# Performance work log

Hardware: AMD Instinct MI355X
Metric: run time of the kernel (lower is better)

Reference implementation:

```python
import jax, jax.numpy as jnp
import numpy as np

N = 50000      # number of predictions
E = 1_600_000  # total neighborhood entries (sum of neighborhood sizes)
D = 128        # prediction representation dim
A = 4          # additional per-pair info dim (box offsets / IoU)
H = 128        # block hidden dim


def setup_inputs() -> dict:
    key = jax.random.key(0)
    ks = jax.random.split(key, 16)
    interpolated = jax.random.normal(ks[0], (N, D), dtype=jnp.float32)
    add_info = jax.random.normal(ks[1], (E, A), dtype=jnp.float32)
    neighbor_idx = jax.random.randint(ks[2], (E,), 0, N, dtype=jnp.int32)
    segment_ids = jnp.sort(jax.random.randint(ks[3], (E,), 0, N, dtype=jnp.int32))
    w = lambda k, shape: (jax.random.normal(k, shape, dtype=jnp.float32) * 0.02)
    return {
        "interpolated": interpolated,
        "add_info": add_info,
        "neighbor_idx": neighbor_idx,
        "segment_ids": segment_ids,
        "Wb0": w(ks[4], (D + A, H)), "bb0": jnp.zeros((H,), jnp.float32),
        "Wo0": w(ks[5], (H, D)),     "bo0": jnp.zeros((D,), jnp.float32),
        "Wb1": w(ks[6], (D + A, H)), "bb1": jnp.zeros((H,), jnp.float32),
        "Wo1": w(ks[7], (H, D)),     "bo1": jnp.zeros((D,), jnp.float32),
        "Wf": w(ks[8], (D, 1)),      "bf": jnp.zeros((1,), jnp.float32),
    }


def reference(interpolated, add_info, neighbor_idx, segment_ids,
              Wb0, bb0, Wo0, bo0, Wb1, bb1, Wo1, bo1, Wf, bf):
    def block_step(feats, Wb, bb, Wo, bo):
        # assemble all neighborhoods: gather neighbor reps, concat pair info -> (E, D+A)
        edge_feats = jnp.concatenate([feats[neighbor_idx], add_info], axis=-1)
        # block MLP on neighborhood entries -> (E, H)
        h = jax.nn.relu(edge_feats @ Wb + bb)
        # segment-wise max pool over each prediction's neighborhood -> (N, H)
        pooled = jax.ops.segment_max(h, segment_ids, num_segments=N)
        pooled = jnp.where(jnp.isfinite(pooled), pooled, 0.0)  # empty segments -> 0
        # output projection back to representation space, residual update
        return feats + (pooled @ Wo + bo)

    x = block_step(interpolated, Wb0, bb0, Wo0, bo0)
    x = block_step(x, Wb1, bb1, Wo1, bo1)
    # final layers: compress representation to updated objectness score -> (N, 1)
    return x @ Wf + bf
```

## Files before the change

### kernel.cpp

```cpp
#include <hip/hip_runtime.h>
#include <limits.h>
#include <cstdint>

typedef __bf16 bf16_t;
typedef __attribute__((ext_vector_type(8))) __bf16 bf16x8;
typedef __attribute__((ext_vector_type(4))) float f32x4;
typedef __attribute__((ext_vector_type(2))) float f32x2;

#define CH 64

__device__ __forceinline__ float rlf(float v, int l) {
  return __int_as_float(__builtin_amdgcn_readlane(__float_as_int(v), l));
}

struct PackArgs {
  const float* W[4];
  bf16_t* P[4];
};

__global__ __launch_bounds__(256) void pack4_kernel(PackArgs args) {
  int idx = blockIdx.x * blockDim.x + threadIdx.x;
  int which = idx >> 14;
  int r = idx & 16383;
  int j  = r & 7;
  int L  = (r >> 3) & 63;
  int nt = (r >> 9) & 7;
  int kt = r >> 12;
  int k = kt * 32 + (L >> 4) * 8 + j;
  int n = nt * 16 + (L & 15);
  args.P[which][r] = (bf16_t)args.W[which][(size_t)k * 128 + n];
}

__global__ __launch_bounds__(256, 4) void yproj_f32(
    const float* __restrict__ X, const bf16_t* __restrict__ Wtpk,
    bf16_t* __restrict__ Ybf, float* __restrict__ pooled, int N)
{
  const int tid = threadIdx.x;
  const int base = blockIdx.x * 128;

  float4 z = make_float4(0.f, 0.f, 0.f, 0.f);
  #pragma unroll
  for (int i = 0; i < 16; ++i) {
    int idx = tid + i * 256;
    int row = base + (idx >> 5);
    if (row < N)
      reinterpret_cast<float4*>(pooled)[(size_t)row * 32 + (idx & 31)] = z;
  }

  const int lane = tid & 63;
  const int w    = tid >> 6;
  const int q    = lane >> 4;
  const int ln   = lane & 15;
  const int n0   = base + w * 32;

  int r0 = n0 + ln, r1 = n0 + 16 + ln;
  int r0c = (r0 < N) ? r0 : (N - 1);
  int r1c = (r1 < N) ? r1 : (N - 1);
  const float* x0 = X + (size_t)r0c * 128 + q * 8;
  const float* x1 = X + (size_t)r1c * 128 + q * 8;

  f32x4 acc[2][8];
  #pragma unroll
  for (int mt = 0; mt < 2; ++mt)
    #pragma unroll
    for (int nt = 0; nt < 8; ++nt)
      #pragma unroll
      for (int r = 0; r < 4; ++r) acc[mt][nt][r] = 0.f;

  const bf16x8* Wp = reinterpret_cast<const bf16x8*>(Wtpk);
  #pragma unroll
  for (int kt = 0; kt < 4; ++kt) {
    float4 f0a = *reinterpret_cast<const float4*>(x0 + kt * 32);
    float4 f0b = *reinterpret_cast<const float4*>(x0 + kt * 32 + 4);
    float4 f1a = *reinterpret_cast<const float4*>(x1 + kt * 32);
    float4 f1b = *reinterpret_cast<const float4*>(x1 + kt * 32 + 4);
    bf16x8 a0, a1;
    a0[0] = (bf16_t)f0a.x; a0[1] = (bf16_t)f0a.y; a0[2] = (bf16_t)f0a.z; a0[3] = (bf16_t)f0a.w;
    a0[4] = (bf16_t)f0b.x; a0[5] = (bf16_t)f0b.y; a0[6] = (bf16_t)f0b.z; a0[7] = (bf16_t)f0b.w;
    a1[0] = (bf16_t)f1a.x; a1[1] = (bf16_t)f1a.y; a1[2] = (bf16_t)f1a.z; a1[3] = (bf16_t)f1a.w;
    a1[4] = (bf16_t)f1b.x; a1[5] = (bf16_t)f1b.y; a1[6] = (bf16_t)f1b.z; a1[7] = (bf16_t)f1b.w;
    #pragma unroll
    for (int nt = 0; nt < 8; ++nt) {
      bf16x8 bfrag = Wp[(kt * 8 + nt) * 64 + lane];
      acc[0][nt] = __builtin_amdgcn_mfma_f32_16x16x32_bf16(a0, bfrag, acc[0][nt], 0, 0, 0);
      acc[1][nt] = __builtin_amdgcn_mfma_f32_16x16x32_bf16(a1, bfrag, acc[1][nt], 0, 0, 0);
    }
  }

  #pragma unroll
  for (int mt = 0; mt < 2; ++mt) {
    #pragma unroll
    for (int r = 0; r < 4; ++r) {
      int row = n0 + mt * 16 + q * 4 + r;
      if (row < N) {
        #pragma unroll
        for (int nt = 0; nt < 8; ++nt) {
          int col = nt * 16 + ln;
          Ybf[(size_t)row * 128 + col] = (bf16_t)acc[mt][nt][r];
        }
      }
    }
  }
}

__global__ __launch_bounds__(256, 4) void yproj_bf16(
    const bf16_t* __restrict__ Xbf, const bf16_t* __restrict__ Wtpk,
    bf16_t* __restrict__ Ybf, float* __restrict__ pooled, int N)
{
  const int tid = threadIdx.x;
  const int base = blockIdx.x * 128;

  float4 z = make_float4(0.f, 0.f, 0.f, 0.f);
  #pragma unroll
  for (int i = 0; i < 16; ++i) {
    int idx = tid + i * 256;
    int row = base + (idx >> 5);
    if (row < N)
      reinterpret_cast<float4*>(pooled)[(size_t)row * 32 + (idx & 31)] = z;
  }

  const int lane = tid & 63;
  const int w    = tid >> 6;
  const int q    = lane >> 4;
  const int ln   = lane & 15;
  const int n0   = base + w * 32;

  int r0 = n0 + ln, r1 = n0 + 16 + ln;
  int r0c = (r0 < N) ? r0 : (N - 1);
  int r1c = (r1 < N) ? r1 : (N - 1);
  const bf16_t* x0 = Xbf + (size_t)r0c * 128 + q * 8;
  const bf16_t* x1 = Xbf + (size_t)r1c * 128 + q * 8;

  f32x4 acc[2][8];
  #pragma unroll
  for (int mt = 0; mt < 2; ++mt)
    #pragma unroll
    for (int nt = 0; nt < 8; ++nt)
      #pragma unroll
      for (int r = 0; r < 4; ++r) acc[mt][nt][r] = 0.f;

  const bf16x8* Wp = reinterpret_cast<const bf16x8*>(Wtpk);
  #pragma unroll
  for (int kt = 0; kt < 4; ++kt) {
    bf16x8 a0 = *reinterpret_cast<const bf16x8*>(x0 + kt * 32);
    bf16x8 a1 = *reinterpret_cast<const bf16x8*>(x1 + kt * 32);
    #pragma unroll
    for (int nt = 0; nt < 8; ++nt) {
      bf16x8 bfrag = Wp[(kt * 8 + nt) * 64 + lane];
      acc[0][nt] = __builtin_amdgcn_mfma_f32_16x16x32_bf16(a0, bfrag, acc[0][nt], 0, 0, 0);
      acc[1][nt] = __builtin_amdgcn_mfma_f32_16x16x32_bf16(a1, bfrag, acc[1][nt], 0, 0, 0);
    }
  }

  #pragma unroll
  for (int mt = 0; mt < 2; ++mt) {
    #pragma unroll
    for (int r = 0; r < 4; ++r) {
      int row = n0 + mt * 16 + q * 4 + r;
      if (row < N) {
        #pragma unroll
        for (int nt = 0; nt < 8; ++nt) {
          int col = nt * 16 + ln;
          Ybf[(size_t)row * 128 + col] = (bf16_t)acc[mt][nt][r];
        }
      }
    }
  }
}

__global__ __launch_bounds__(256) void edge_stream(
    const bf16_t* __restrict__ Y,
    const float* __restrict__ Wb,
    const float* __restrict__ bb,
    const float* __restrict__ add_info,
    const int* __restrict__ nbr, const int* __restrict__ segs,
    float* __restrict__ pooled, int E)
{
  const int lane = threadIdx.x & 63;
  const int wv = __builtin_amdgcn_readfirstlane(threadIdx.x >> 6);
  const int e0 = (blockIdx.x * 4 + wv) * CH;
  if (e0 >= E) return;
  const int c0 = lane * 2;

  f32x2 wk[4];
  #pragma unroll
  for (int k = 0; k < 4; ++k) {
    wk[k].x = Wb[(size_t)(128 + k) * 128 + c0];
    wk[k].y = Wb[(size_t)(128 + k) * 128 + c0 + 1];
  }
  f32x2 bbv;
  bbv.x = bb[c0]; bbv.y = bb[c0 + 1];

  unsigned* pooled_u = reinterpret_cast<unsigned*>(pooled);
  f32x2 v; v.x = 0.f; v.y = 0.f;

  if (e0 + CH <= E) {
    int v_nbr = nbr[e0 + lane];
    int v_sg  = segs[e0 + lane];
    float v_ai[4];
    #pragma unroll
    for (int r = 0; r < 4; ++r)
      v_ai[r] = add_info[(size_t)e0 * 4 + r * 64 + lane];

    int cur = __builtin_amdgcn_readlane(v_sg, 0);

    unsigned ybuf[4][8];
    #pragma unroll
    for (int p = 0; p < 3; ++p) {
      #pragma unroll
      for (int j = 0; j < 8; ++j) {
        int rn = __builtin_amdgcn_readlane(v_nbr, p * 8 + j);
        ybuf[p][j] = *((const unsigned*)(Y + (size_t)rn * 128) + lane);
      }
    }

    #pragma unroll
    for (int g = 0; g < CH / 8; ++g) {
      if (g + 3 < CH / 8) {
        #pragma unroll
        for (int j = 0; j < 8; ++j) {
          int rn = __builtin_amdgcn_readlane(v_nbr, (g + 3) * 8 + j);
          ybuf[(g + 3) & 3][j] = *((const unsigned*)(Y + (size_t)rn * 128) + lane);
        }
      }
      #pragma unroll
      for (int j = 0; j < 8; ++j) {
        const int i = g * 8 + j;
        int sg = __builtin_amdgcn_readlane(v_sg, i);
        if (sg != cur) {
          if (v.x > 0.f) atomicMax(&pooled_u[(size_t)cur * 128 + c0], __float_as_uint(v.x));
          if (v.y > 0.f) atomicMax(&pooled_u[(size_t)cur * 128 + c0 + 1], __float_as_uint(v.y));
          v.x = 0.f; v.y = 0.f; cur = sg;
        }
        unsigned yb = ybuf[g & 3][j];
        f32x2 y;
        y.x = __uint_as_float(yb << 16);
        y.y = __uint_as_float(yb & 0xffff0000u);
        float a0 = rlf(v_ai[i >> 4], (i * 4 + 0) & 63);
        float a1 = rlf(v_ai[i >> 4], (i * 4 + 1) & 63);
        float a2 = rlf(v_ai[i >> 4], (i * 4 + 2) & 63);
        float a3 = rlf(v_ai[i >> 4], (i * 4 + 3) & 63);
        f32x2 t = bbv + a0 * wk[0];
        t += a1 * wk[1];
        t += a2 * wk[2];
        t += a3 * wk[3];
        t += y;
        v = __builtin_elementwise_max(v, t);
      }
    }
    if (v.x > 0.f) atomicMax(&pooled_u[(size_t)cur * 128 + c0], __float_as_uint(v.x));
    if (v.y > 0.f) atomicMax(&pooled_u[(size_t)cur * 128 + c0 + 1], __float_as_uint(v.y));
  } else {
    int cur = segs[e0];
    const int rem = E - e0;
    for (int i = 0; i < rem; ++i) {
      const int e = e0 + i;
      int sg = segs[e];
      if (sg != cur) {
        if (v.x > 0.f) atomicMax(&pooled_u[(size_t)cur * 128 + c0], __float_as_uint(v.x));
        if (v.y > 0.f) atomicMax(&pooled_u[(size_t)cur * 128 + c0 + 1], __float_as_uint(v.y));
        v.x = 0.f; v.y = 0.f; cur = sg;
      }
      unsigned yb = *reinterpret_cast<const unsigned*>(Y + (size_t)nbr[e] * 128 + c0);
      float y0 = __uint_as_float(yb << 16);
      float y1 = __uint_as_float(yb & 0xffff0000u);
      const float* ai = add_info + (size_t)e * 4;
      float a0 = ai[0], a1 = ai[1], a2 = ai[2], a3 = ai[3];
      float t0 = y0 + bbv.x + a0 * wk[0].x + a1 * wk[1].x + a2 * wk[2].x + a3 * wk[3].x;
      float t1 = y1 + bbv.y + a0 * wk[0].y + a1 * wk[1].y + a2 * wk[2].y + a3 * wk[3].y;
      v.x = fmaxf(v.x, t0);
      v.y = fmaxf(v.y, t1);
    }
    if (v.x > 0.f) atomicMax(&pooled_u[(size_t)cur * 128 + c0], __float_as_uint(v.x));
    if (v.y > 0.f) atomicMax(&pooled_u[(size_t)cur * 128 + c0 + 1], __float_as_uint(v.y));
  }
}

__global__ __launch_bounds__(256, 4) void update_mfma(
    const float* __restrict__ featsIn, const float* __restrict__ pooled,
    const bf16_t* __restrict__ Wopk, const float* __restrict__ bo,
    float* __restrict__ featsOut, bf16_t* __restrict__ featsOutBf, int N)
{
  const int tid  = threadIdx.x;
  const int lane = tid & 63;
  const int w    = tid >> 6;
  const int q    = lane >> 4;
  const int ln   = lane & 15;
  const int n0   = blockIdx.x * 128 + w * 32;

  int r0 = n0 + ln, r1 = n0 + 16 + ln;
  int r0c = (r0 < N) ? r0 : (N - 1);
  int r1c = (r1 < N) ? r1 : (N - 1);
  const float* p0 = pooled + (size_t)r0c * 128 + q * 8;
  const float* p1 = pooled + (size_t)r1c * 128 + q * 8;

  f32x4 acc[2][8];
  #pragma unroll
  for (int mt = 0; mt < 2; ++mt)
    #pragma unroll
    for (int nt = 0; nt < 8; ++nt)
      #pragma unroll
      for (int r = 0; r < 4; ++r) acc[mt][nt][r] = 0.f;

  const bf16x8* Wp = reinterpret_cast<const bf16x8*>(Wopk);
  #pragma unroll
  for (int kt = 0; kt < 4; ++kt) {
    float4 f0a = *reinterpret_cast<const float4*>(p0 + kt * 32);
    float4 f0b = *reinterpret_cast<const float4*>(p0 + kt * 32 + 4);
    float4 f1a = *reinterpret_cast<const float4*>(p1 + kt * 32);
    float4 f1b = *reinterpret_cast<const float4*>(p1 + kt * 32 + 4);
    bf16x8 a0, a1;
    a0[0] = (bf16_t)f0a.x; a0[1] = (bf16_t)f0a.y; a0[2] = (bf16_t)f0a.z; a0[3] = (bf16_t)f0a.w;
    a0[4] = (bf16_t)f0b.x; a0[5] = (bf16_t)f0b.y; a0[6] = (bf16_t)f0b.z; a0[7] = (bf16_t)f0b.w;
    a1[0] = (bf16_t)f1a.x; a1[1] = (bf16_t)f1a.y; a1[2] = (bf16_t)f1a.z; a1[3] = (bf16_t)f1a.w;
    a1[4] = (bf16_t)f1b.x; a1[5] = (bf16_t)f1b.y; a1[6] = (bf16_t)f1b.z; a1[7] = (bf16_t)f1b.w;
    #pragma unroll
    for (int nt = 0; nt < 8; ++nt) {
      bf16x8 bfrag = Wp[(kt * 8 + nt) * 64 + lane];
      acc[0][nt] = __builtin_amdgcn_mfma_f32_16x16x32_bf16(a0, bfrag, acc[0][nt], 0, 0, 0);
      acc[1][nt] = __builtin_amdgcn_mfma_f32_16x16x32_bf16(a1, bfrag, acc[1][nt], 0, 0, 0);
    }
  }

  float bov[8];
  #pragma unroll
  for (int nt = 0; nt < 8; ++nt) bov[nt] = bo[nt * 16 + ln];

  #pragma unroll
  for (int mt = 0; mt < 2; ++mt) {
    #pragma unroll
    for (int r = 0; r < 4; ++r) {
      int row = n0 + mt * 16 + q * 4 + r;
      if (row < N) {
        #pragma unroll
        for (int nt = 0; nt < 8; ++nt) {
          int col = nt * 16 + ln;
          float o = featsIn[(size_t)row * 128 + col] + acc[mt][nt][r] + bov[nt];
          featsOut[(size_t)row * 128 + col] = o;
          featsOutBf[(size_t)row * 128 + col] = (bf16_t)o;
        }
      }
    }
  }
}

__global__ __launch_bounds__(256, 4) void update_final_mfma(
    const float* __restrict__ featsIn, const float* __restrict__ pooled,
    const bf16_t* __restrict__ Wopk, const float* __restrict__ bo,
    const float* __restrict__ Wf, const float* __restrict__ bf_,
    float* __restrict__ out, int N)
{
  const int tid  = threadIdx.x;
  const int lane = tid & 63;
  const int w    = tid >> 6;
  const int q    = lane >> 4;
  const int ln   = lane & 15;
  const int n0   = blockIdx.x * 128 + w * 32;

  int r0 = n0 + ln, r1 = n0 + 16 + ln;
  int r0c = (r0 < N) ? r0 : (N - 1);
  int r1c = (r1 < N) ? r1 : (N - 1);
  const float* p0 = pooled + (size_t)r0c * 128 + q * 8;
  const float* p1 = pooled + (size_t)r1c * 128 + q * 8;

  f32x4 acc[2][8];
  #pragma unroll
  for (int mt = 0; mt < 2; ++mt)
    #pragma unroll
    for (int nt = 0; nt < 8; ++nt)
      #pragma unroll
      for (int r = 0; r < 4; ++r) acc[mt][nt][r] = 0.f;

  const bf16x8* Wp = reinterpret_cast<const bf16x8*>(Wopk);
  #pragma unroll
  for (int kt = 0; kt < 4; ++kt) {
    float4 f0a = *reinterpret_cast<const float4*>(p0 + kt * 32);
    float4 f0b = *reinterpret_cast<const float4*>(p0 + kt * 32 + 4);
    float4 f1a = *reinterpret_cast<const float4*>(p1 + kt * 32);
    float4 f1b = *reinterpret_cast<const float4*>(p1 + kt * 32 + 4);
    bf16x8 a0, a1;
    a0[0] = (bf16_t)f0a.x; a0[1] = (bf16_t)f0a.y; a0[2] = (bf16_t)f0a.z; a0[3] = (bf16_t)f0a.w;
    a0[4] = (bf16_t)f0b.x; a0[5] = (bf16_t)f0b.y; a0[6] = (bf16_t)f0b.z; a0[7] = (bf16_t)f0b.w;
    a1[0] = (bf16_t)f1a.x; a1[1] = (bf16_t)f1a.y; a1[2] = (bf16_t)f1a.z; a1[3] = (bf16_t)f1a.w;
    a1[4] = (bf16_t)f1b.x; a1[5] = (bf16_t)f1b.y; a1[6] = (bf16_t)f1b.z; a1[7] = (bf16_t)f1b.w;
    #pragma unroll
    for (int nt = 0; nt < 8; ++nt) {
      bf16x8 bfrag = Wp[(kt * 8 + nt) * 64 + lane];
      acc[0][nt] = __builtin_amdgcn_mfma_f32_16x16x32_bf16(a0, bfrag, acc[0][nt], 0, 0, 0);
      acc[1][nt] = __builtin_amdgcn_mfma_f32_16x16x32_bf16(a1, bfrag, acc[1][nt], 0, 0, 0);
    }
  }

  float bov[8], wfv[8];
  #pragma unroll
  for (int nt = 0; nt < 8; ++nt) { bov[nt] = bo[nt * 16 + ln]; wfv[nt] = Wf[nt * 16 + ln]; }
  float bfs = bf_[0];

  #pragma unroll
  for (int mt = 0; mt < 2; ++mt) {
    #pragma unroll
    for (int r = 0; r < 4; ++r) {
      int row = n0 + mt * 16 + q * 4 + r;
      float partial = 0.f;
      if (row < N) {
        #pragma unroll
        for (int nt = 0; nt < 8; ++nt) {
          int col = nt * 16 + ln;
          float o = featsIn[(size_t)row * 128 + col] + acc[mt][nt][r] + bov[nt];
          partial += o * wfv[nt];
        }
      }
      partial += __shfl_xor(partial, 1);
      partial += __shfl_xor(partial, 2);
      partial += __shfl_xor(partial, 4);
      partial += __shfl_xor(partial, 8);
      if (ln == 0 && row < N) out[row] = partial + bfs;
    }
  }
}

extern "C" void kernel_launch(void* const* d_in, const int* in_sizes, int n_in,
                              void* d_out, int out_size, void* d_ws, size_t ws_size,
                              hipStream_t stream)
{
  const float* interpolated = (const float*)d_in[0];
  const float* add_info     = (const float*)d_in[1];
  const int*   nbr          = (const int*)d_in[2];
  const int*   segs         = (const int*)d_in[3];
  const float* Wb0 = (const float*)d_in[4];
  const float* bb0 = (const float*)d_in[5];
  const float* Wo0 = (const float*)d_in[6];
  const float* bo0 = (const float*)d_in[7];
  const float* Wb1 = (const float*)d_in[8];
  const float* bb1 = (const float*)d_in[9];
  const float* Wo1 = (const float*)d_in[10];
  const float* bo1 = (const float*)d_in[11];
  const float* Wf  = (const float*)d_in[12];
  const float* bf_ = (const float*)d_in[13];

  const int N = in_sizes[0] / 128;
  const int E = in_sizes[2];
  float* out = (float*)d_out;

  float* pooled = (float*)d_ws;
  float* featsB = pooled + (size_t)N * 128;
  bf16_t* featsB_bf = (bf16_t*)(featsB + (size_t)N * 128);
  bf16_t* Ybf       = featsB_bf + (size_t)N * 128;
  bf16_t* Wtpk0 = Ybf + (size_t)N * 128;
  bf16_t* Wtpk1 = Wtpk0 + 16384;
  bf16_t* Wopk0 = Wtpk1 + 16384;
  bf16_t* Wopk1 = Wopk0 + 16384;

  const int ugrid = (N + 127) / 128;
  const int egrid = (E + CH * 4 - 1) / (CH * 4);

  PackArgs pa;
  pa.W[0] = Wb0; pa.P[0] = Wtpk0;
  pa.W[1] = Wb1; pa.P[1] = Wtpk1;
  pa.W[2] = Wo0; pa.P[2] = Wopk0;
  pa.W[3] = Wo1; pa.P[3] = Wopk1;
  pack4_kernel<<<256, 256, 0, stream>>>(pa);

  yproj_f32<<<ugrid, 256, 0, stream>>>(interpolated, Wtpk0, Ybf, pooled, N);
  edge_stream<<<egrid, 256, 0, stream>>>(Ybf, Wb0, bb0, add_info, nbr, segs,
                                         pooled, E);
  update_mfma<<<ugrid, 256, 0, stream>>>(interpolated, pooled, Wopk0, bo0,
                                         featsB, featsB_bf, N);

  yproj_bf16<<<ugrid, 256, 0, stream>>>(featsB_bf, Wtpk1, Ybf, pooled, N);
  edge_stream<<<egrid, 256, 0, stream>>>(Ybf, Wb1, bb1, add_info, nbr, segs,
                                         pooled, E);
  update_final_mfma<<<ugrid, 256, 0, stream>>>(featsB, pooled, Wopk1, bo1,
                                               Wf, bf_, out, N);
}
```

Before: 306.5 us.

## Stage neighbor gathers through LDS via global_load_lds with explicit vmcnt pipeline

Replaces the register-buffered gather of neighbor Y rows with direct global-to-LDS loads into a four-deep per-wave ring buffer, with hand-placed vmcnt waits so up to 32 row loads stay in flight. Segment boundaries are precomputed once as a ballot bitmask instead of a per-edge readlane and compare. The aim is to raise memory-level parallelism on the random gathers and free the VGPRs the ring held. The cost is 32KB of LDS per block, which may limit occupancy, and it relies on hand-set waitcnt values and LDS reads that must match the hardware's completion order.

```diff
diff --git a/kernel.cpp b/kernel.cpp
--- a/kernel.cpp
+++ b/kernel.cpp
@@ -8,6 +8,9 @@
 typedef __attribute__((ext_vector_type(2))) float f32x2;
 
 #define CH 64
+
+typedef const __attribute__((address_space(1))) unsigned GU;
+typedef __attribute__((address_space(3))) unsigned LU;
 
 __device__ __forceinline__ float rlf(float v, int l) {
   return __int_as_float(__builtin_amdgcn_readlane(__float_as_int(v), l));
@@ -168,6 +171,50 @@
   }
 }
 
+#define EGROUP(G, WAITN)                                                      \
+  {                                                                           \
+    asm volatile("s_waitcnt vmcnt(" WAITN ")" ::: "memory");                  \
+    __builtin_amdgcn_sched_barrier(0);                                        \
+    unsigned yv[8];                                                           \
+    _Pragma("unroll")                                                         \
+    for (int j = 0; j < 8; ++j) yv[j] = y_lds[wv][(G) & 3][j][lane];          \
+    asm volatile("s_waitcnt lgkmcnt(0)" ::: "memory");                        \
+    __builtin_amdgcn_sched_barrier(0);                                        \
+    if ((G) + 4 < 8) {                                                        \
+      _Pragma("unroll")                                                       \
+      for (int j = 0; j < 8; ++j) {                                           \
+        int rn = __builtin_amdgcn_readlane(v_nbr, ((G) + 4) * 8 + j);         \
+        const unsigned* src = (const unsigned*)(Y + (size_t)rn * 128) + lane; \
+        __builtin_amdgcn_global_load_lds((GU*)(const void*)src,               \
+            (LU*)(void*)&y_lds[wv][(G) & 3][j][0], 4, 0, 0);                  \
+      }                                                                       \
+    }                                                                         \
+    _Pragma("unroll")                                                         \
+    for (int j = 0; j < 8; ++j) {                                             \
+      const int i = (G) * 8 + j;                                              \
+      if (bmask & (1ull << i)) {                                              \
+        if (v.x > 0.f) atomicMax(&pooled_u[(size_t)cur * 128 + c0], __float_as_uint(v.x));      \
+        if (v.y > 0.f) atomicMax(&pooled_u[(size_t)cur * 128 + c0 + 1], __float_as_uint(v.y));  \
+        v.x = 0.f; v.y = 0.f;                                                 \
+        cur = __builtin_amdgcn_readlane(v_sg, i);                             \
+      }                                                                       \
+      unsigned yb = yv[j];                                                    \
+      f32x2 y;                                                                \
+      y.x = __uint_as_float(yb << 16);                                        \
+      y.y = __uint_as_float(yb & 0xffff0000u);                                \
+      float a0 = rlf(v_ai[i >> 4], (i * 4 + 0) & 63);                         \
+      float a1 = rlf(v_ai[i >> 4], (i * 4 + 1) & 63);                         \
+      float a2 = rlf(v_ai[i >> 4], (i * 4 + 2) & 63);                         \
+      float a3 = rlf(v_ai[i >> 4], (i * 4 + 3) & 63);                         \
+      f32x2 t = bbv + a0 * wk[0];                                             \
+      t += a1 * wk[1];                                                        \
+      t += a2 * wk[2];                                                        \
+      t += a3 * wk[3];                                                        \
+      t += y;                                                                 \
+      v = __builtin_elementwise_max(v, t);                                    \
+    }                                                                         \
+  }
+
 __global__ __launch_bounds__(256) void edge_stream(
     const bf16_t* __restrict__ Y,
     const float* __restrict__ Wb,
@@ -176,6 +223,7 @@
     const int* __restrict__ nbr, const int* __restrict__ segs,
     float* __restrict__ pooled, int E)
 {
+  __shared__ unsigned y_lds[4][4][8][64];
   const int lane = threadIdx.x & 63;
   const int wv = __builtin_amdgcn_readfirstlane(threadIdx.x >> 6);
   const int e0 = (blockIdx.x * 4 + wv) * CH;
@@ -202,52 +250,30 @@
     for (int r = 0; r < 4; ++r)
       v_ai[r] = add_info[(size_t)e0 * 4 + r * 64 + lane];
 
+    int sg_prev = __shfl_up(v_sg, 1);
+    unsigned long long bmask = __ballot(v_sg != sg_prev) & ~1ull;
     int cur = __builtin_amdgcn_readlane(v_sg, 0);
 
-    unsigned ybuf[4][8];
-    #pragma unroll
-    for (int p = 0; p < 3; ++p) {
+    #pragma unroll
+    for (int p = 0; p < 4; ++p) {
       #pragma unroll
       for (int j = 0; j < 8; ++j) {
         int rn = __builtin_amdgcn_readlane(v_nbr, p * 8 + j);
-        ybuf[p][j] = *((const unsigned*)(Y + (size_t)rn * 128) + lane);
+        const unsigned* src = (const unsigned*)(Y + (size_t)rn * 128) + lane;
+        __builtin_amdgcn_global_load_lds((GU*)(const void*)src,
+            (LU*)(void*)&y_lds[wv][p][j][0], 4, 0, 0);
       }
     }
 
-    #pragma unroll
-    for (int g = 0; g < CH / 8; ++g) {
-      if (g + 3 < CH / 8) {
-        #pragma unroll
-        for (int j = 0; j < 8; ++j) {
-          int rn = __builtin_amdgcn_readlane(v_nbr, (g + 3) * 8 + j);
-          ybuf[(g + 3) & 3][j] = *((const unsigned*)(Y + (size_t)rn * 128) + lane);
-        }
-      }
-      #pragma unroll
-      for (int j = 0; j < 8; ++j) {
-        const int i = g * 8 + j;
-        int sg = __builtin_amdgcn_readlane(v_sg, i);
-        if (sg != cur) {
-          if (v.x > 0.f) atomicMax(&pooled_u[(size_t)cur * 128 + c0], __float_as_uint(v.x));
-          if (v.y > 0.f) atomicMax(&pooled_u[(size_t)cur * 128 + c0 + 1], __float_as_uint(v.y));
-          v.x = 0.f; v.y = 0.f; cur = sg;
-        }
-        unsigned yb = ybuf[g & 3][j];
-        f32x2 y;
-        y.x = __uint_as_float(yb << 16);
-        y.y = __uint_as_float(yb & 0xffff0000u);
-        float a0 = rlf(v_ai[i >> 4], (i * 4 + 0) & 63);
-        float a1 = rlf(v_ai[i >> 4], (i * 4 + 1) & 63);
-        float a2 = rlf(v_ai[i >> 4], (i * 4 + 2) & 63);
-        float a3 = rlf(v_ai[i >> 4], (i * 4 + 3) & 63);
-        f32x2 t = bbv + a0 * wk[0];
-        t += a1 * wk[1];
-        t += a2 * wk[2];
-        t += a3 * wk[3];
-        t += y;
-        v = __builtin_elementwise_max(v, t);
-      }
-    }
+    EGROUP(0, "24")
+    EGROUP(1, "24")
+    EGROUP(2, "24")
+    EGROUP(3, "24")
+    EGROUP(4, "24")
+    EGROUP(5, "16")
+    EGROUP(6, "8")
+    EGROUP(7, "0")
+
     if (v.x > 0.f) atomicMax(&pooled_u[(size_t)cur * 128 + c0], __float_as_uint(v.x));
     if (v.y > 0.f) atomicMax(&pooled_u[(size_t)cur * 128 + c0 + 1], __float_as_uint(v.y));
   } else {
```

Measured after the change: 305.8 us. Within noise of the previous version (-0.2%).
